# Kernel tuning notes

Hardware: AMD Instinct MI355X
Metric: run time of the kernel (lower is better)

Reference implementation:

```python
import jax, jax.numpy as jnp
import numpy as np

EPS = 1e-12  # torch F.normalize eps

def _l2norm(x, axis):
    n = jnp.linalg.norm(x, axis=axis, keepdims=True)
    return x / jnp.maximum(n, EPS)

def setup_inputs() -> dict:
    key = jax.random.key(0)
    ks = jax.random.split(key, 4)
    B, T, C, E, I = 2, 2048, 1024, 8, 2048
    return {
        "hidden_states": jax.random.normal(ks[0], (B, T, C), dtype=jnp.float32),
        "sim_matrix": jax.random.normal(ks[1], (C, E), dtype=jnp.float32),
        "gates": jnp.zeros((E,), dtype=jnp.float32),
        "temperature": jnp.float32(1.0),
        "experts_mask": jnp.ones((E,), dtype=jnp.float32),
        "w1": jax.random.normal(ks[2], (E, C, I), dtype=jnp.float32) * (1.0 / np.sqrt(C)),
        "w2": jax.random.normal(ks[3], (E, I, C), dtype=jnp.float32) * (1.0 / np.sqrt(I)),
        "min_experts": 2,
    }

def _gating(flat_h, sim_matrix, gates, temperature, experts_mask, min_experts):
    # flat_h: [N, C]
    logit_scale = jax.nn.sigmoid(temperature)
    logits = _l2norm(flat_h, -1) @ _l2norm(sim_matrix, 0)  # [N, E]
    logits = logits * experts_mask
    gated = jax.nn.relu(logits - gates * logit_scale)
    # GateSTE: forward hard threshold, backward identity
    act = gated + jax.lax.stop_gradient((gated > 0).astype(gated.dtype) - gated)
    # fallback: tokens with no active expert get top-min_experts by logits
    inactive = jnp.sum(act, axis=1) == 0  # [N]
    _, idx = jax.lax.top_k(logits, min_experts)  # [N, k]
    fallback = jnp.sum(jax.nn.one_hot(idx, logits.shape[1], dtype=act.dtype), axis=1) > 0  # [N, E] bool
    act = jnp.where(inactive[:, None] & fallback, jnp.asarray(1.0, act.dtype), act)
    return act, logits

def reference(hidden_states, sim_matrix, gates, temperature, experts_mask, w1, w2, min_experts):
    b, t, c = hidden_states.shape
    e = w1.shape[0]
    act, router_logits = _gating(hidden_states.reshape(b * t, c), sim_matrix, gates,
                                 temperature, experts_mask, min_experts)
    inter = jnp.einsum('btc,eci->btei', hidden_states, w1)
    inter = jax.nn.gelu(inter, approximate=False)
    expert_out = jnp.einsum('btei,eic->btec', inter, w2)
    mask = act.reshape(b, t, e)
    summed = jnp.sum(expert_out * mask[..., None], axis=-2)  # [b,t,c]
    num_act = jnp.clip(jnp.sum(mask, axis=-1, keepdims=True), 1, None)
    final = summed / num_act
    return final, router_logits, act
```

## Files before the change

### kernel.cpp

```cpp
#include <hip/hip_runtime.h>
#include <math.h>

typedef __bf16 bf16x8 __attribute__((ext_vector_type(8)));
typedef __bf16 bf16x4 __attribute__((ext_vector_type(4)));
typedef float  f32x4  __attribute__((ext_vector_type(4)));

#define NTOK 4096
#define CDIM 1024
#define EEXP 8
#define IDIM 2048

__device__ __forceinline__ void async_copy16(const __bf16* g, __bf16* l) {
  __builtin_amdgcn_global_load_lds((const __attribute__((address_space(1))) void*)g,
                                   (__attribute__((address_space(3))) void*)l,
                                   16, 0, 0);
}

__device__ __forceinline__ float gelu_f(float x) {
  float u = 0.7978845608028654f * fmaf(0.044715f * x * x, x, x);
  float ex = __expf(-2.f * fabsf(u));
  float th = copysignf((1.f - ex) / (1.f + ex), u);
  return 0.5f * x * (1.f + th);
}

__global__ __launch_bounds__(256) void gating_kernel(
    const float* __restrict__ h, const float* __restrict__ sim,
    const float* __restrict__ gates, const float* __restrict__ temp,
    const float* __restrict__ emask, const int* __restrict__ minexp,
    float* __restrict__ out_logits, float* __restrict__ out_act,
    float* __restrict__ inv_num, __bf16* __restrict__ hb)
{
  const int t = blockIdx.x, tid = threadIdx.x;
  float4 hv4 = ((const float4*)(h + (size_t)t * CDIM))[tid];
  float hv[4] = {hv4.x, hv4.y, hv4.z, hv4.w};
  bf16x4 hb4 = {(__bf16)hv[0], (__bf16)hv[1], (__bf16)hv[2], (__bf16)hv[3]};
  ((bf16x4*)(hb + (size_t)t * CDIM))[tid] = hb4;

  float d[EEXP], nn[EEXP];
  #pragma unroll
  for (int e = 0; e < EEXP; ++e) { d[e] = 0.f; nn[e] = 0.f; }
  float ss = 0.f;
  #pragma unroll
  for (int j = 0; j < 4; ++j) {
    ss = fmaf(hv[j], hv[j], ss);
    const float* sr = sim + (size_t)(tid * 4 + j) * EEXP;
    float4 s0 = ((const float4*)sr)[0];
    float4 s1 = ((const float4*)sr)[1];
    float sv[8] = {s0.x, s0.y, s0.z, s0.w, s1.x, s1.y, s1.z, s1.w};
    #pragma unroll
    for (int e = 0; e < EEXP; ++e) {
      d[e]  = fmaf(hv[j], sv[e], d[e]);
      nn[e] = fmaf(sv[e], sv[e], nn[e]);
    }
  }
  #pragma unroll
  for (int off = 32; off > 0; off >>= 1) {
    ss += __shfl_down(ss, off);
    #pragma unroll
    for (int e = 0; e < EEXP; ++e) {
      d[e]  += __shfl_down(d[e], off);
      nn[e] += __shfl_down(nn[e], off);
    }
  }
  __shared__ float red[4][20];
  const int wv = tid >> 6;
  if ((tid & 63) == 0) {
    red[wv][0] = ss;
    #pragma unroll
    for (int e = 0; e < EEXP; ++e) { red[wv][1 + e] = d[e]; red[wv][9 + e] = nn[e]; }
  }
  __syncthreads();
  if (tid == 0) {
    float sst = red[0][0] + red[1][0] + red[2][0] + red[3][0];
    float inv_h = 1.f / fmaxf(sqrtf(sst), 1e-12f);
    float ls = 1.f / (1.f + expf(-temp[0]));
    float logit[EEXP], act[EEXP];
    float cnt = 0.f;
    #pragma unroll
    for (int e = 0; e < EEXP; ++e) {
      float dot = red[0][1 + e] + red[1][1 + e] + red[2][1 + e] + red[3][1 + e];
      float nne = red[0][9 + e] + red[1][9 + e] + red[2][9 + e] + red[3][9 + e];
      float inv_s = 1.f / fmaxf(sqrtf(nne), 1e-12f);
      logit[e] = dot * inv_h * inv_s * emask[e];
      float g = logit[e] - gates[e] * ls;
      act[e] = (g > 0.f) ? 1.f : 0.f;
      cnt += act[e];
    }
    if (cnt == 0.f) {
      int k = minexp[0];
      if (k > EEXP) k = EEXP;
      bool used[EEXP];
      #pragma unroll
      for (int e = 0; e < EEXP; ++e) used[e] = false;
      for (int j = 0; j < k; ++j) {
        int best = -1; float bv = 0.f;
        for (int e = 0; e < EEXP; ++e)
          if (!used[e] && (best < 0 || logit[e] > bv)) { best = e; bv = logit[e]; }
        if (best >= 0) { used[best] = true; act[best] = 1.f; cnt += 1.f; }
      }
    }
    float num = fmaxf(cnt, 1.f);
    inv_num[t] = 1.f / num;
    #pragma unroll
    for (int e = 0; e < EEXP; ++e) {
      out_logits[(size_t)t * EEXP + e] = logit[e];
      out_act[(size_t)t * EEXP + e]   = act[e];
    }
  }
}

__global__ __launch_bounds__(64) void pack_kernel(
    const float* __restrict__ out_act, int* __restrict__ counts,
    unsigned short* __restrict__ perm)
{
  const int e = blockIdx.x;
  const int lane = threadIdx.x;
  const unsigned long long ltmask = (lane == 63) ? ~0ULL >> 1 : (1ULL << lane) - 1ULL;
  int base = 0;
  for (int i = 0; i < NTOK / 64; ++i) {
    int tok = i * 64 + lane;
    bool f = out_act[(size_t)tok * EEXP + e] > 0.f;
    unsigned long long m = __ballot(f);
    if (f) perm[e * NTOK + base + __popcll(m & ltmask)] = (unsigned short)tok;
    base += __popcll(m);
  }
  if (lane == 0) counts[e] = base;
}

__global__ __launch_bounds__(256) void transpose_f32_bf16(
    const float* __restrict__ in0, __bf16* __restrict__ out0, int R, int Cc,
    long sIn, long sOut)
{
  const float* in = in0 + (size_t)blockIdx.z * sIn;
  __bf16* out = out0 + (size_t)blockIdx.z * sOut;
  __shared__ __align__(16) __bf16 tile[64][72];
  const int tid = threadIdx.x;
  const int c0 = blockIdx.x * 64, r0 = blockIdx.y * 64;
  #pragma unroll
  for (int p = 0; p < 2; ++p) {
    int lin = p * 256 + tid;
    int r = lin >> 3, c8 = (lin & 7) * 8;
    const float* src = in + (size_t)(r0 + r) * Cc + c0 + c8;
    float4 v0 = ((const float4*)src)[0];
    float4 v1 = ((const float4*)src)[1];
    bf16x8 v = {(__bf16)v0.x, (__bf16)v0.y, (__bf16)v0.z, (__bf16)v0.w,
                (__bf16)v1.x, (__bf16)v1.y, (__bf16)v1.z, (__bf16)v1.w};
    *(bf16x8*)&tile[r][c8] = v;
  }
  __syncthreads();
  #pragma unroll
  for (int p = 0; p < 2; ++p) {
    int lin = p * 256 + tid;
    int oc = lin >> 3, j8 = (lin & 7) * 8;
    bf16x8 o;
    #pragma unroll
    for (int jj = 0; jj < 8; ++jj) o[jj] = tile[j8 + jj][oc];
    *(bf16x8*)(out + (size_t)(c0 + oc) * R + r0 + j8) = o;
  }
}

template <int MODE, int NN, int KK, int NB>
__global__ __launch_bounds__(512, 2) void gemm_pk(
    const __bf16* __restrict__ A0, const __bf16* __restrict__ B0,
    const int* __restrict__ counts, const unsigned short* __restrict__ perm,
    const float* __restrict__ inv_num, void* __restrict__ Cout)
{
  const int hid = blockIdx.x;
  const int xr = hid & 7, q = hid >> 3;
  const int mb = q & 15;
  const int panel = ((q >> 4) << 3) + xr;
  const int e = panel / NB;
  const int nb = panel - e * NB;
  const int Me = counts[e];
  const int m0 = mb * 256;
  if (m0 >= Me) return;
  const int n0 = nb * 256;

  const int tid = threadIdx.x;
  const int wave = tid >> 6, lane = tid & 63;
  const int wr = wave >> 2, wc = wave & 3;
  const int quad = lane >> 4, lrow = lane & 15;
  const int axk = ((quad ^ (lrow & 3)) << 3);

  __shared__ __align__(16) __bf16 lds[4 * 16384];
  #define LDSA(j) (lds + (((j) & 3) << 14))
  #define LDSB(j) (lds + (((j) & 3) << 14) + 8192)

  const int lr = tid >> 2;
  const int ch = ((tid & 3) ^ (lr & 3)) << 3;
  const unsigned short* pe = perm + e * NTOK;
  const __bf16 *aS0, *aS1;
  if (MODE == 0) {
    aS0 = A0 + (size_t)pe[min(m0 + lr, Me - 1)] * KK + ch;
    aS1 = A0 + (size_t)pe[min(m0 + 128 + lr, Me - 1)] * KK + ch;
  } else {
    const __bf16* Ab = A0 + (size_t)e * NTOK * KK;
    aS0 = Ab + (size_t)(m0 + lr) * KK + ch;
    aS1 = Ab + (size_t)(m0 + 128 + lr) * KK + ch;
  }
  const __bf16* Bb = B0 + (size_t)e * ((size_t)CDIM * IDIM);
  const __bf16* bS0 = Bb + (size_t)(n0 + lr) * KK + ch;
  const __bf16* bS1 = Bb + (size_t)(n0 + 128 + lr) * KK + ch;

  f32x4 acc[8][4] = {};
  constexpr int NS = KK / 32;

  async_copy16(aS0,      LDSA(0) + wave * 512);
  async_copy16(aS1,      LDSA(0) + 4096 + wave * 512);
  async_copy16(bS0,      LDSB(0) + wave * 512);
  async_copy16(bS1,      LDSB(0) + 4096 + wave * 512);
  async_copy16(aS0 + 32, LDSA(1) + wave * 512);
  async_copy16(aS1 + 32, LDSA(1) + 4096 + wave * 512);
  async_copy16(bS0 + 32, LDSB(1) + wave * 512);
  async_copy16(bS1 + 32, LDSB(1) + 4096 + wave * 512);
  asm volatile("s_waitcnt vmcnt(4)" ::: "memory");
  __builtin_amdgcn_s_barrier();

  const int arow = (wr << 7) + lrow;
  const int brow = (wc << 6) + lrow;

  for (int s = 0; s < NS; ++s) {
    const __bf16* Asl = LDSA(s);
    const __bf16* Bsl = LDSB(s);
    bf16x8 af[4], bfr[4];
    #pragma unroll
    for (int mi = 0; mi < 4; ++mi)
      af[mi] = *(const bf16x8*)(Asl + ((arow + mi * 16) << 5) + axk);
    #pragma unroll
    for (int ni = 0; ni < 4; ++ni)
      bfr[ni] = *(const bf16x8*)(Bsl + ((brow + ni * 16) << 5) + axk);
    if (s + 2 < NS) {
      async_copy16(aS0 + (s + 2) * 32, LDSA(s + 2) + wave * 512);
      async_copy16(aS1 + (s + 2) * 32, LDSA(s + 2) + 4096 + wave * 512);
    }
    __builtin_amdgcn_s_barrier();
    __builtin_amdgcn_s_setprio(1);
    #pragma unroll
    for (int mi = 0; mi < 4; ++mi)
      #pragma unroll
      for (int ni = 0; ni < 4; ++ni)
        acc[mi][ni] = __builtin_amdgcn_mfma_f32_16x16x32_bf16(af[mi], bfr[ni], acc[mi][ni], 0, 0, 0);
    __builtin_amdgcn_s_setprio(0);
    __builtin_amdgcn_s_barrier();
    #pragma unroll
    for (int mi = 0; mi < 4; ++mi)
      af[mi] = *(const bf16x8*)(Asl + ((arow + 64 + mi * 16) << 5) + axk);
    if (s + 2 < NS) {
      async_copy16(bS0 + (s + 2) * 32, LDSB(s + 2) + wave * 512);
      async_copy16(bS1 + (s + 2) * 32, LDSB(s + 2) + 4096 + wave * 512);
    }
    __builtin_amdgcn_s_barrier();
    __builtin_amdgcn_s_setprio(1);
    #pragma unroll
    for (int mi = 0; mi < 4; ++mi)
      #pragma unroll
      for (int ni = 0; ni < 4; ++ni)
        acc[4 + mi][ni] = __builtin_amdgcn_mfma_f32_16x16x32_bf16(af[mi], bfr[ni], acc[4 + mi][ni], 0, 0, 0);
    __builtin_amdgcn_s_setprio(0);
    if (s + 2 < NS)      { asm volatile("s_waitcnt vmcnt(4)" ::: "memory"); }
    else if (s + 1 < NS) { asm volatile("s_waitcnt vmcnt(0)" ::: "memory"); }
    __builtin_amdgcn_s_barrier();
  }
  #undef LDSA
  #undef LDSB

  if (MODE == 0) {
    __bf16* O = (__bf16*)Cout + (size_t)e * NTOK * NN;
    #pragma unroll
    for (int mi = 0; mi < 8; ++mi) {
      #pragma unroll
      for (int r = 0; r < 4; ++r) {
        const int row = m0 + (wr << 7) + mi * 16 + (quad << 2) + r;
        const float sv = inv_num[pe[min(row, Me - 1)]];
        #pragma unroll
        for (int ni = 0; ni < 4; ++ni) {
          const int col = n0 + (wc << 6) + ni * 16 + lrow;
          O[(size_t)row * NN + col] = (__bf16)(gelu_f(acc[mi][ni][r]) * sv);
        }
      }
    }
  } else {
    float* O = (float*)Cout;
    #pragma unroll
    for (int mi = 0; mi < 8; ++mi) {
      #pragma unroll
      for (int r = 0; r < 4; ++r) {
        const int row = m0 + (wr << 7) + mi * 16 + (quad << 2) + r;
        if (row < Me) {
          const int tok = pe[row];
          #pragma unroll
          for (int ni = 0; ni < 4; ++ni) {
            const int col = n0 + (wc << 6) + ni * 16 + lrow;
            atomicAdd(&O[(size_t)tok * NN + col], acc[mi][ni][r]);
          }
        }
      }
    }
  }
}

extern "C" void kernel_launch(void* const* d_in, const int* in_sizes, int n_in,
                              void* d_out, int out_size, void* d_ws, size_t ws_size,
                              hipStream_t stream) {
  (void)in_sizes; (void)n_in; (void)out_size; (void)ws_size;
  const float* h     = (const float*)d_in[0];
  const float* sim   = (const float*)d_in[1];
  const float* gates = (const float*)d_in[2];
  const float* temp  = (const float*)d_in[3];
  const float* emask = (const float*)d_in[4];
  const float* w1    = (const float*)d_in[5];
  const float* w2    = (const float*)d_in[6];
  const int*   minexp = (const int*)d_in[7];

  float* out_final  = (float*)d_out;
  float* out_logits = out_final + (size_t)NTOK * CDIM;
  float* out_act    = out_logits + (size_t)NTOK * EEXP;

  char* ws = (char*)d_ws;
  float*          inv_num  = (float*)(ws + 0);
  int*            counts   = (int*)(ws + 16384);
  unsigned short* perm     = (unsigned short*)(ws + 16448);
  __bf16*         hb       = (__bf16*)(ws + 81984);
  __bf16*         w1T_all  = (__bf16*)(ws + 8470592);
  __bf16*         w2T_all  = (__bf16*)(ws + 42025024);
  __bf16*         inter_pk = (__bf16*)(ws + 75579456);

  const long sW = (long)CDIM * IDIM;

  hipMemsetAsync(out_final, 0, (size_t)NTOK * CDIM * sizeof(float), stream);
  transpose_f32_bf16<<<dim3(IDIM / 64, CDIM / 64, EEXP), 256, 0, stream>>>(
      w1, w1T_all, CDIM, IDIM, sW, sW);
  transpose_f32_bf16<<<dim3(CDIM / 64, IDIM / 64, EEXP), 256, 0, stream>>>(
      w2, w2T_all, IDIM, CDIM, sW, sW);
  gating_kernel<<<NTOK, 256, 0, stream>>>(h, sim, gates, temp, emask, minexp,
                                          out_logits, out_act, inv_num, hb);
  pack_kernel<<<EEXP, 64, 0, stream>>>(out_act, counts, perm);
  gemm_pk<0, IDIM, CDIM, IDIM / 256><<<dim3((IDIM / 256) * (NTOK / 256) * EEXP), 512, 0, stream>>>(
      hb, w1T_all, counts, perm, inv_num, (void*)inter_pk);
  gemm_pk<1, CDIM, IDIM, CDIM / 256><<<dim3((CDIM / 256) * (NTOK / 256) * EEXP), 512, 0, stream>>>(
      inter_pk, w2T_all, counts, perm, inv_num, (void*)out_final);
}
```

Before: 509.3 us.

## Use 64-wide K tiles with double-buffered LDS and one barrier per step

The expert GEMM main loop moves from 32-wide K slices in a four-slot ring, prefetched two steps ahead with several barriers per step, to 64-wide K slices in two LDS buffers prefetched one step ahead. Each iteration now does a single wait and barrier, and the XOR swizzle widens to 8 chunks to match the 64-element rows. The aim is to halve loop iterations and cut barrier and synchronisation overhead. In exchange, prefetch distance shrinks to one stage and each step fully drains outstanding loads, so global-load latency may be less well hidden.

```diff
diff --git a/kernel.cpp b/kernel.cpp
--- a/kernel.cpp
+++ b/kernel.cpp
@@ -166,9 +166,9 @@
     const float* __restrict__ inv_num, void* __restrict__ Cout)
 {
   const int hid = blockIdx.x;
-  const int xr = hid & 7, q = hid >> 3;
-  const int mb = q & 15;
-  const int panel = ((q >> 4) << 3) + xr;
+  const int xr = hid & 7, q2 = hid >> 3;
+  const int mb = q2 & 15;
+  const int panel = ((q2 >> 4) << 3) + xr;
   const int e = panel / NB;
   const int nb = panel - e * NB;
   const int Me = counts[e];
@@ -180,89 +180,90 @@
   const int wave = tid >> 6, lane = tid & 63;
   const int wr = wave >> 2, wc = wave & 3;
   const int quad = lane >> 4, lrow = lane & 15;
-  const int axk = ((quad ^ (lrow & 3)) << 3);
-
-  __shared__ __align__(16) __bf16 lds[4 * 16384];
-  #define LDSA(j) (lds + (((j) & 3) << 14))
-  #define LDSB(j) (lds + (((j) & 3) << 14) + 8192)
-
-  const int lr = tid >> 2;
-  const int ch = ((tid & 3) ^ (lr & 3)) << 3;
+  const int sw0 = ((quad ^ (lrow & 7)) << 3);
+  const int sw1 = (((4 + quad) ^ (lrow & 7)) << 3);
+
+  __shared__ __align__(16) __bf16 lds[2 * 32768];
+
+  const int lr2 = tid >> 3;
+  const int ch  = (((tid & 7) ^ (lr2 & 7)) << 3);
   const unsigned short* pe = perm + e * NTOK;
-  const __bf16 *aS0, *aS1;
+  const __bf16* aP[4];
+  const __bf16* bP[4];
   if (MODE == 0) {
-    aS0 = A0 + (size_t)pe[min(m0 + lr, Me - 1)] * KK + ch;
-    aS1 = A0 + (size_t)pe[min(m0 + 128 + lr, Me - 1)] * KK + ch;
+    #pragma unroll
+    for (int g = 0; g < 4; ++g)
+      aP[g] = A0 + (size_t)pe[min(m0 + g * 64 + lr2, Me - 1)] * KK + ch;
   } else {
     const __bf16* Ab = A0 + (size_t)e * NTOK * KK;
-    aS0 = Ab + (size_t)(m0 + lr) * KK + ch;
-    aS1 = Ab + (size_t)(m0 + 128 + lr) * KK + ch;
+    #pragma unroll
+    for (int g = 0; g < 4; ++g)
+      aP[g] = Ab + (size_t)(m0 + g * 64 + lr2) * KK + ch;
   }
   const __bf16* Bb = B0 + (size_t)e * ((size_t)CDIM * IDIM);
-  const __bf16* bS0 = Bb + (size_t)(n0 + lr) * KK + ch;
-  const __bf16* bS1 = Bb + (size_t)(n0 + 128 + lr) * KK + ch;
+  #pragma unroll
+  for (int g = 0; g < 4; ++g)
+    bP[g] = Bb + (size_t)(n0 + g * 64 + lr2) * KK + ch;
 
   f32x4 acc[8][4] = {};
-  constexpr int NS = KK / 32;
-
-  async_copy16(aS0,      LDSA(0) + wave * 512);
-  async_copy16(aS1,      LDSA(0) + 4096 + wave * 512);
-  async_copy16(bS0,      LDSB(0) + wave * 512);
-  async_copy16(bS1,      LDSB(0) + 4096 + wave * 512);
-  async_copy16(aS0 + 32, LDSA(1) + wave * 512);
-  async_copy16(aS1 + 32, LDSA(1) + 4096 + wave * 512);
-  async_copy16(bS0 + 32, LDSB(1) + wave * 512);
-  async_copy16(bS1 + 32, LDSB(1) + 4096 + wave * 512);
-  asm volatile("s_waitcnt vmcnt(4)" ::: "memory");
+  constexpr int NS = KK / 64;
+
+  {
+    __bf16* slot = lds;
+    #pragma unroll
+    for (int g = 0; g < 4; ++g)
+      async_copy16(aP[g], slot + g * 4096 + wave * 512);
+    #pragma unroll
+    for (int g = 0; g < 4; ++g)
+      async_copy16(bP[g], slot + 16384 + g * 4096 + wave * 512);
+  }
+  asm volatile("s_waitcnt vmcnt(0)" ::: "memory");
   __builtin_amdgcn_s_barrier();
 
-  const int arow = (wr << 7) + lrow;
-  const int brow = (wc << 6) + lrow;
+  const int arow0 = (wr << 7) + lrow;
+  const int brow0 = (wc << 6) + lrow;
 
   for (int s = 0; s < NS; ++s) {
-    const __bf16* Asl = LDSA(s);
-    const __bf16* Bsl = LDSB(s);
-    bf16x8 af[4], bfr[4];
-    #pragma unroll
-    for (int mi = 0; mi < 4; ++mi)
-      af[mi] = *(const bf16x8*)(Asl + ((arow + mi * 16) << 5) + axk);
-    #pragma unroll
-    for (int ni = 0; ni < 4; ++ni)
-      bfr[ni] = *(const bf16x8*)(Bsl + ((brow + ni * 16) << 5) + axk);
-    if (s + 2 < NS) {
-      async_copy16(aS0 + (s + 2) * 32, LDSA(s + 2) + wave * 512);
-      async_copy16(aS1 + (s + 2) * 32, LDSA(s + 2) + 4096 + wave * 512);
-    }
-    __builtin_amdgcn_s_barrier();
-    __builtin_amdgcn_s_setprio(1);
-    #pragma unroll
-    for (int mi = 0; mi < 4; ++mi)
+    if (s + 1 < NS) {
+      __bf16* slot = lds + (((s + 1) & 1) << 15);
+      const int ko = (s + 1) * 64;
+      #pragma unroll
+      for (int g = 0; g < 4; ++g)
+        async_copy16(aP[g] + ko, slot + g * 4096 + wave * 512);
+      #pragma unroll
+      for (int g = 0; g < 4; ++g)
+        async_copy16(bP[g] + ko, slot + 16384 + g * 4096 + wave * 512);
+    }
+    const __bf16* Asl = lds + ((s & 1) << 15);
+    const __bf16* Bsl = Asl + 16384;
+    #pragma unroll
+    for (int kh = 0; kh < 2; ++kh) {
+      const int sw = kh ? sw1 : sw0;
+      bf16x8 bfr[4];
       #pragma unroll
       for (int ni = 0; ni < 4; ++ni)
-        acc[mi][ni] = __builtin_amdgcn_mfma_f32_16x16x32_bf16(af[mi], bfr[ni], acc[mi][ni], 0, 0, 0);
-    __builtin_amdgcn_s_setprio(0);
-    __builtin_amdgcn_s_barrier();
-    #pragma unroll
-    for (int mi = 0; mi < 4; ++mi)
-      af[mi] = *(const bf16x8*)(Asl + ((arow + 64 + mi * 16) << 5) + axk);
-    if (s + 2 < NS) {
-      async_copy16(bS0 + (s + 2) * 32, LDSB(s + 2) + wave * 512);
-      async_copy16(bS1 + (s + 2) * 32, LDSB(s + 2) + 4096 + wave * 512);
-    }
-    __builtin_amdgcn_s_barrier();
-    __builtin_amdgcn_s_setprio(1);
-    #pragma unroll
-    for (int mi = 0; mi < 4; ++mi)
-      #pragma unroll
-      for (int ni = 0; ni < 4; ++ni)
-        acc[4 + mi][ni] = __builtin_amdgcn_mfma_f32_16x16x32_bf16(af[mi], bfr[ni], acc[4 + mi][ni], 0, 0, 0);
-    __builtin_amdgcn_s_setprio(0);
-    if (s + 2 < NS)      { asm volatile("s_waitcnt vmcnt(4)" ::: "memory"); }
-    else if (s + 1 < NS) { asm volatile("s_waitcnt vmcnt(0)" ::: "memory"); }
-    __builtin_amdgcn_s_barrier();
-  }
-  #undef LDSA
-  #undef LDSB
+        bfr[ni] = *(const bf16x8*)(Bsl + ((brow0 + ni * 16) << 6) + sw);
+      #pragma unroll
+      for (int mh = 0; mh < 2; ++mh) {
+        bf16x8 af[4];
+        #pragma unroll
+        for (int mi = 0; mi < 4; ++mi)
+          af[mi] = *(const bf16x8*)(Asl + ((arow0 + (mh * 4 + mi) * 16) << 6) + sw);
+        __builtin_amdgcn_s_setprio(1);
+        #pragma unroll
+        for (int mi = 0; mi < 4; ++mi)
+          #pragma unroll
+          for (int ni = 0; ni < 4; ++ni)
+            acc[mh * 4 + mi][ni] =
+                __builtin_amdgcn_mfma_f32_16x16x32_bf16(af[mi], bfr[ni], acc[mh * 4 + mi][ni], 0, 0, 0);
+        __builtin_amdgcn_s_setprio(0);
+      }
+    }
+    if (s + 1 < NS) {
+      asm volatile("s_waitcnt vmcnt(0)" ::: "memory");
+      __builtin_amdgcn_s_barrier();
+    }
+  }
 
   if (MODE == 0) {
     __bf16* O = (__bf16*)Cout + (size_t)e * NTOK * NN;
```

Result: no change. 500.4 us (-1.7%).
